# Kernel optimization log

Hardware: AMD Instinct MI355X
Metric: run time of the kernel (lower is better)

The kernel has to match this reference:

```python
import jax, jax.numpy as jnp
import numpy as np

HIDDEN = 1024
N_HEADS = 16
N_KV = 4
HEAD_DIM = HIDDEN // N_HEADS  # 64


def setup_inputs() -> dict:
    key = jax.random.key(0)
    ks = jax.random.split(key, 10)
    B, S, D = 2, 2048, HIDDEN
    s = 0.02
    return {
        "hidden_states": jax.random.normal(ks[0], (B, S, D), jnp.float32),
        "attention_mask": jnp.ones((B, S), jnp.float32),
        "Wq": jax.random.normal(ks[1], (D, N_HEADS * HEAD_DIM), jnp.float32) * s,
        "bq": jnp.zeros((N_HEADS * HEAD_DIM,), jnp.float32),
        "Wk": jax.random.normal(ks[2], (D, N_KV * HEAD_DIM), jnp.float32) * s,
        "bk": jnp.zeros((N_KV * HEAD_DIM,), jnp.float32),
        "Wv": jax.random.normal(ks[3], (D, N_KV * HEAD_DIM), jnp.float32) * s,
        "bv": jnp.zeros((N_KV * HEAD_DIM,), jnp.float32),
        "Wo": jax.random.normal(ks[4], (D, D), jnp.float32) * s,
        "bo": jnp.zeros((D,), jnp.float32),
    }


def _rope(x):
    # x: [B, H, S, Dh]; half-split RoPE as in the torch module
    S, Dh = x.shape[-2], x.shape[-1]
    inv_freq = 1.0 / (10000.0 ** (jnp.arange(0, Dh, 2, dtype=jnp.float32) / Dh))
    freqs = jnp.arange(S, dtype=jnp.float32)[:, None] * inv_freq[None, :]  # [S, Dh/2]
    cos, sin = jnp.cos(freqs), jnp.sin(freqs)
    x1, x2 = jnp.split(x, 2, axis=-1)
    return jnp.concatenate([x1 * cos - x2 * sin, x1 * sin + x2 * cos], axis=-1)


def reference(hidden_states, attention_mask, Wq, bq, Wk, bk, Wv, bv, Wo, bo):
    B, S, D = hidden_states.shape
    q = (hidden_states @ Wq + bq).reshape(B, S, N_HEADS, HEAD_DIM).transpose(0, 2, 1, 3)
    k = (hidden_states @ Wk + bk).reshape(B, S, N_KV, HEAD_DIM).transpose(0, 2, 1, 3)
    v = (hidden_states @ Wv + bv).reshape(B, S, N_KV, HEAD_DIM).transpose(0, 2, 1, 3)
    q = _rope(q)
    k = _rope(k)
    rep = N_HEADS // N_KV
    k = jnp.repeat(k, rep, axis=1)  # [B, H, S, Dh]
    v = jnp.repeat(v, rep, axis=1)
    bias = (1.0 - attention_mask[:, None, None, :]) * -1e9  # [B,1,1,S]
    scores = jnp.einsum("bhqd,bhkd->bhqk", q, k) / jnp.sqrt(jnp.float32(HEAD_DIM))
    attn = jax.nn.softmax(scores + bias, axis=-1)
    out = jnp.einsum("bhqk,bhkd->bhqd", attn, v)
    out = out.transpose(0, 2, 1, 3).reshape(B, S, D)
    return out @ Wo + bo
```

## Files before the change

kernel.cpp:

```cpp
#include <hip/hip_runtime.h>

typedef __bf16 bf16;
typedef __attribute__((ext_vector_type(8))) __bf16 bf16x8;
typedef __attribute__((ext_vector_type(4))) __bf16 bf16x4;
typedef __attribute__((ext_vector_type(4))) float f32x4;
typedef __attribute__((ext_vector_type(16))) float f32x16;
typedef __attribute__((ext_vector_type(4))) unsigned int uint4v;

#define LOG2E 1.44269504088896340736f
#define QSCALE 0.18033688011112042f

__device__ inline void tr_tile(const float* __restrict__ in, bf16* __restrict__ out,
                               int R, int C, int bx, int by, int tid) {
    __shared__ float t[32][33];
    int tx = tid & 31, ty = tid >> 5;
    int rbase = by * 32, cbase = bx * 32;
#pragma unroll
    for (int i = 0; i < 4; i++) {
        int r = ty + i * 8;
        t[r][tx] = in[(size_t)(rbase + r) * C + cbase + tx];
    }
    __syncthreads();
#pragma unroll
    for (int i = 0; i < 4; i++) {
        int r = ty + i * 8;
        out[(size_t)(cbase + r) * R + rbase + tx] = (bf16)t[tx][r];
    }
}

__global__ __launch_bounds__(256) void prep_k(const float* __restrict__ X,
                                              const float* __restrict__ Wq,
                                              const float* __restrict__ Wk,
                                              const float* __restrict__ Wv,
                                              const float* __restrict__ Wo,
                                              const float* __restrict__ mask,
                                              bf16* __restrict__ Xb,
                                              bf16* __restrict__ WqT,
                                              bf16* __restrict__ WkT,
                                              bf16* __restrict__ WvT,
                                              bf16* __restrict__ WoT,
                                              float2* __restrict__ rt,
                                              float* __restrict__ Mb,
                                              int* __restrict__ mflags) {
    int blk = blockIdx.x, tid = threadIdx.x;
    if (blk < 2048) {
        int idx = (blk * 256 + tid) * 8;
        float4 a = *(const float4*)(X + idx);
        float4 b = *(const float4*)(X + idx + 4);
        bf16 v[8] = {(bf16)a.x, (bf16)a.y, (bf16)a.z, (bf16)a.w,
                     (bf16)b.x, (bf16)b.y, (bf16)b.z, (bf16)b.w};
        *(uint4*)(Xb + idx) = *(const uint4*)v;
    } else if (blk < 3072) {
        int t = blk - 2048; tr_tile(Wq, WqT, 1024, 1024, t & 31, t >> 5, tid);
    } else if (blk < 3328) {
        int t = blk - 3072; tr_tile(Wk, WkT, 1024, 256, t & 7, t >> 3, tid);
    } else if (blk < 3584) {
        int t = blk - 3328; tr_tile(Wv, WvT, 1024, 256, t & 7, t >> 3, tid);
    } else if (blk < 4608) {
        int t = blk - 3584; tr_tile(Wo, WoT, 1024, 1024, t & 31, t >> 5, tid);
    } else if (blk < 4864) {
        int idx = (blk - 4608) * 256 + tid;
        int s = idx >> 5, i = idx & 31;
        float inv = exp2f(-0.41524100370589830f * (float)i);
        float ang = (float)s * inv;
        rt[idx] = make_float2(cosf(ang), sinf(ang));
    } else {
        __shared__ int sflag;
        int b = blk - 4864;
        if (tid == 0) sflag = 1;
        __syncthreads();
        const float* mrow = mask + (size_t)b * 2048;
        int i0 = tid * 8;
        bool ones = true;
#pragma unroll
        for (int j = 0; j < 8; j++) {
            float m = mrow[i0 + j];
            if (m != 1.0f) ones = false;
            Mb[(size_t)b * 2048 + i0 + j] = (1.0f - m) * (-1e9f) * LOG2E;
        }
        if (!ones) sflag = 0;
        __syncthreads();
        if (tid == 0) mflags[b] = sflag;
    }
}

__device__ __forceinline__ void gemm_main_db(bf16* __restrict__ pool,
                                             const bf16* __restrict__ A,
                                             const bf16* __restrict__ BT,
                                             int m0, int n0, int tid,
                                             f32x4 (&acc)[2][8]) {
    int w = tid >> 6, lane = tid & 63, l15 = lane & 15, quad = lane >> 4;

    int srow = lane >> 3;
    int kx = ((lane & 7) ^ srow) * 8;
    const bf16* ga0 = A + (size_t)(m0 + w * 32 + srow) * 1024 + kx;
    const bf16* gb0 = BT + (size_t)(n0 + w * 32 + srow) * 1024 + kx;
    int lofs = (w * 32) * 64 + lane * 8;

#define GSTAGE(K0, BUF)                                                                             \
    do {                                                                                            \
        bf16* gbase = pool + (BUF) * 16384;                                                         \
        _Pragma("unroll")                                                                           \
        for (int p = 0; p < 4; p++)                                                                 \
            __builtin_amdgcn_global_load_lds(                                                       \
                (const __attribute__((address_space(1))) unsigned int*)(ga0 + (size_t)p * 8 * 1024 + (K0)), \
                (__attribute__((address_space(3))) unsigned int*)(gbase + lofs + p * 512), 16, 0, 0); \
        _Pragma("unroll")                                                                           \
        for (int p = 0; p < 4; p++)                                                                 \
            __builtin_amdgcn_global_load_lds(                                                       \
                (const __attribute__((address_space(1))) unsigned int*)(gb0 + (size_t)p * 8 * 1024 + (K0)), \
                (__attribute__((address_space(3))) unsigned int*)(gbase + 8192 + lofs + p * 512), 16, 0, 0); \
    } while (0)

    GSTAGE(0, 0);
    __syncthreads();

    for (int ks = 0; ks < 16; ks++) {
        int cb = ks & 1;
        if (ks < 15) GSTAGE((ks + 1) * 64, cb ^ 1);
        const bf16* As = pool + cb * 16384;
        const bf16* Bs = As + 8192;
#pragma unroll
        for (int half = 0; half < 2; half++) {
            bf16x8 a[2], bfr[8];
            int kp = ((half * 4 + quad) ^ (l15 & 7)) * 8;
#pragma unroll
            for (int i = 0; i < 2; i++)
                a[i] = *(const bf16x8*)&As[(w * 32 + i * 16 + l15) * 64 + kp];
#pragma unroll
            for (int j = 0; j < 8; j++)
                bfr[j] = *(const bf16x8*)&Bs[(j * 16 + l15) * 64 + kp];
#pragma unroll
            for (int i = 0; i < 2; i++)
#pragma unroll
                for (int j = 0; j < 8; j++)
                    acc[i][j] = __builtin_amdgcn_mfma_f32_16x16x32_bf16(a[i], bfr[j], acc[i][j], 0, 0, 0);
        }
        __syncthreads();
    }
#undef GSTAGE
}

__global__ __launch_bounds__(256, 2) void qkv_gemm2(const bf16* __restrict__ Xb,
                                                    const bf16* __restrict__ WTall,
                                                    const float* __restrict__ bq,
                                                    const float* __restrict__ bk,
                                                    const float* __restrict__ bv,
                                                    const float2* __restrict__ rt,
                                                    bf16* __restrict__ Qb,
                                                    bf16* __restrict__ Kb,
                                                    bf16* __restrict__ VbT) {
    __shared__ __align__(16) bf16 pool[2 * 16384];
    int tt = blockIdx.x, gy = blockIdx.y, tid = threadIdx.x;
    f32x4 acc[2][8] = {};
    gemm_main_db(pool, Xb, WTall, tt * 128, gy * 128, tid, acc);

    int w = tid >> 6, lane = tid & 63, l15 = lane & 15, quad = lane >> 4;

    if (gy >= 10) {
        int kvb = (gy - 10) * 2;
        bf16* T = pool;
#pragma unroll
        for (int i = 0; i < 2; i++)
#pragma unroll
            for (int r = 0; r < 4; r++) {
                int s_local = w * 32 + i * 16 + quad * 4 + r;
#pragma unroll
                for (int j = 0; j < 8; j++) {
                    int dd = j * 16 + l15;
                    T[dd * 136 + s_local] = (bf16)(acc[i][j][r] + bv[kvb * 64 + dd]);
                }
            }
        __syncthreads();
        int dd = tid & 127, sblk = tid >> 7;
        int b = tt >> 4, s_base = (tt & 15) * 128 + sblk * 64;
        int head = kvb + (dd >> 6), d_in = dd & 63;
        const bf16* Trow = T + dd * 136 + sblk * 64;
        size_t orow = ((size_t)(b * 4 + head) * 64 + d_in) * 2048 + s_base;
#pragma unroll
        for (int c = 0; c < 8; c++)
            *(uint4*)(VbT + orow + c * 8) = *(const uint4*)(Trow + c * 8);
        return;
    }

    int mode = (gy < 8) ? 0 : 1;
#pragma unroll
    for (int jh = 0; jh < 2; jh++) {
        int head = (mode == 0) ? gy * 2 + jh : (gy - 8) * 2 + jh;
        const float* bias = ((mode == 0) ? bq : bk) + head * 64;
        bf16* dst = (mode == 0) ? Qb : Kb;
#pragma unroll
        for (int i = 0; i < 2; i++) {
#pragma unroll
            for (int r = 0; r < 4; r++) {
                int token = tt * 128 + w * 32 + i * 16 + quad * 4 + r;
                int b = token >> 11, s = token & 2047;
                float vals[4];
#pragma unroll
                for (int j = 0; j < 4; j++) vals[j] = acc[i][jh * 4 + j][r] + bias[j * 16 + l15];
#pragma unroll
                for (int c = 0; c < 2; c++) {
                    float2 cs2 = rt[s * 32 + c * 16 + l15];
                    float x1 = vals[c], x2 = vals[c + 2];
                    vals[c]     = x1 * cs2.x - x2 * cs2.y;
                    vals[c + 2] = x1 * cs2.y + x2 * cs2.x;
                }
                if (mode == 0) {
#pragma unroll
                    for (int j = 0; j < 4; j++) vals[j] *= QSCALE;
                }
                size_t base;
                if (mode == 0) base = (((size_t)b * 16 + head) * 2048 + s) * 64;
                else           base = (((size_t)b * 4  + head) * 2048 + s) * 64;
#pragma unroll
                for (int j = 0; j < 4; j++) dst[base + j * 16 + l15] = (bf16)vals[j];
            }
        }
    }
}

__global__ __launch_bounds__(256, 2) void oproj_gemm2(const bf16* __restrict__ Ab,
                                                      const bf16* __restrict__ WoT,
                                                      const float* __restrict__ bo,
                                                      float* __restrict__ out) {
    __shared__ __align__(16) bf16 pool[2 * 16384];
    int tt = blockIdx.x, nt = blockIdx.y, tid = threadIdx.x;
    f32x4 acc[2][8] = {};
    gemm_main_db(pool, Ab, WoT, tt * 128, nt * 128, tid, acc);

    int w = tid >> 6, lane = tid & 63, l15 = lane & 15, quad = lane >> 4;
#pragma unroll
    for (int i = 0; i < 2; i++) {
#pragma unroll
        for (int r = 0; r < 4; r++) {
            int token = tt * 128 + w * 32 + i * 16 + quad * 4 + r;
#pragma unroll
            for (int j = 0; j < 8; j++) {
                int n = nt * 128 + j * 16 + l15;
                out[(size_t)token * 1024 + n] = acc[i][j][r] + bo[n];
            }
        }
    }
}

__global__ __launch_bounds__(256, 4) void attn_k(const bf16* __restrict__ Qb,
                                                 const bf16* __restrict__ Kb,
                                                 const bf16* __restrict__ VbT,
                                                 const float* __restrict__ Mb,
                                                 const int* __restrict__ mflags,
                                                 bf16* __restrict__ Opb,
                                                 float* __restrict__ Lp) {
    int qt = blockIdx.x, h = blockIdx.y, z = blockIdx.z;
    int b = z >> 1, sp = z & 1;
    int kvh = h >> 2;
    int kt0 = sp * 16;

    __shared__ bf16 Ks[2][64 * 64];
    __shared__ bf16 Vs[2][64 * 64];

    int tid = threadIdx.x, w = tid >> 6, lane = tid & 63, l31 = lane & 31, hi = lane >> 5;

    const bool maskOnes = (mflags[b] != 0);

    bf16x8 qa[4];
    {
        size_t qrow = (((size_t)b * 16 + h) * 2048 + (size_t)qt * 128 + w * 32 + l31) * 64;
#pragma unroll
        for (int ds = 0; ds < 4; ds++)
            qa[ds] = *(const bf16x8*)(Qb + qrow + ds * 16 + hi * 8);
    }

    f32x16 oacc[2] = {};
    float lsum = 0.f;

    size_t kRow = ((size_t)b * 4 + kvh) * 2048;
    size_t vRow = ((size_t)b * 4 + kvh) * 64;

    int srow = lane >> 3;
    int kx = ((lane & 7) ^ srow) * 8;
    const bf16* gk0 = Kb + (kRow + w * 16 + srow) * 64 + kx;
    const bf16* gv0 = VbT + (vRow + w * 16 + srow) * 2048 + kx;
    int lofs = (w * 16) * 64 + lane * 8;

#define STAGE(KT, BUF)                                                                              \
    do {                                                                                            \
        _Pragma("unroll")                                                                           \
        for (int p = 0; p < 2; p++) {                                                               \
            __builtin_amdgcn_global_load_lds(                                                       \
                (const __attribute__((address_space(1))) unsigned int*)(gk0 + ((size_t)(KT) * 64 + p * 8) * 64), \
                (__attribute__((address_space(3))) unsigned int*)(&Ks[BUF][0] + lofs + p * 512), 16, 0, 0); \
            __builtin_amdgcn_global_load_lds(                                                       \
                (const __attribute__((address_space(1))) unsigned int*)(gv0 + (size_t)p * 8 * 2048 + (KT) * 64), \
                (__attribute__((address_space(3))) unsigned int*)(&Vs[BUF][0] + lofs + p * 512), 16, 0, 0); \
        }                                                                                           \
    } while (0)

    STAGE(kt0, 0);
    __syncthreads();

    const float* mbase = Mb + (size_t)b * 2048 + hi * 4;

    for (int kt = 0; kt < 16; kt++) {
        int cb = kt & 1;
        if (kt < 15) STAGE(kt0 + kt + 1, cb ^ 1);
        int ktg = kt0 + kt;

        const bf16* ksb = &Ks[cb][0];
        const bf16* vsb = &Vs[cb][0];

        uint4v paw[4];
#pragma unroll
        for (int kh = 0; kh < 2; kh++) {
            bf16x8 ka[4];
#pragma unroll
            for (int ds = 0; ds < 4; ds++) {
                int gran = ((ds * 2 + hi) ^ (l31 & 7)) * 8;
                ka[ds] = *(const bf16x8*)&ksb[(kh * 32 + l31) * 64 + gran];
            }
            f32x16 s = {};
#pragma unroll
            for (int ds = 0; ds < 4; ds++)
                s = __builtin_amdgcn_mfma_f32_32x32x16_bf16(ka[ds], qa[ds], s, 0, 0, 0);
            if (!maskOnes) {
#pragma unroll
                for (int g = 0; g < 4; g++) {
                    f32x4 b4 = *(const f32x4*)(mbase + ktg * 64 + kh * 32 + g * 8);
#pragma unroll
                    for (int r = 0; r < 4; r++) s[g * 4 + r] += b4[r];
                }
            }
#pragma unroll
            for (int i = 0; i < 16; i++) { s[i] = exp2f(s[i]); lsum += s[i]; }
            unsigned int d0, d1, d2, d3, d4, d5, d6, d7;
            asm("v_cvt_pk_bf16_f32 %0, %1, %2" : "=v"(d0) : "v"(s[0]),  "v"(s[1]));
            asm("v_cvt_pk_bf16_f32 %0, %1, %2" : "=v"(d1) : "v"(s[2]),  "v"(s[3]));
            asm("v_cvt_pk_bf16_f32 %0, %1, %2" : "=v"(d2) : "v"(s[4]),  "v"(s[5]));
            asm("v_cvt_pk_bf16_f32 %0, %1, %2" : "=v"(d3) : "v"(s[6]),  "v"(s[7]));
            asm("v_cvt_pk_bf16_f32 %0, %1, %2" : "=v"(d4) : "v"(s[8]),  "v"(s[9]));
            asm("v_cvt_pk_bf16_f32 %0, %1, %2" : "=v"(d5) : "v"(s[10]), "v"(s[11]));
            asm("v_cvt_pk_bf16_f32 %0, %1, %2" : "=v"(d6) : "v"(s[12]), "v"(s[13]));
            asm("v_cvt_pk_bf16_f32 %0, %1, %2" : "=v"(d7) : "v"(s[14]), "v"(s[15]));
            asm("v_permlane32_swap_b32 %0, %1" : "+v"(d0), "+v"(d2));
            asm("v_permlane32_swap_b32 %0, %1" : "+v"(d1), "+v"(d3));
            asm("v_permlane32_swap_b32 %0, %1" : "+v"(d4), "+v"(d6));
            asm("v_permlane32_swap_b32 %0, %1" : "+v"(d5), "+v"(d7));
            paw[kh * 2 + 0][0] = d0; paw[kh * 2 + 0][1] = d1;
            paw[kh * 2 + 0][2] = d2; paw[kh * 2 + 0][3] = d3;
            paw[kh * 2 + 1][0] = d4; paw[kh * 2 + 1][1] = d5;
            paw[kh * 2 + 1][2] = d6; paw[kh * 2 + 1][3] = d7;
        }

#pragma unroll
        for (int dg = 0; dg < 2; dg++)
#pragma unroll
            for (int ks = 0; ks < 4; ks++) {
                int gran = ((ks * 2 + hi) ^ (l31 & 7)) * 8;
                bf16x8 vb = *(const bf16x8*)&vsb[(dg * 32 + l31) * 64 + gran];
                oacc[dg] = __builtin_amdgcn_mfma_f32_32x32x16_bf16(
                    __builtin_bit_cast(bf16x8, paw[ks]), vb, oacc[dg], 0, 0, 0);
            }
        __syncthreads();
    }
#undef STAGE

    lsum += __shfl_xor(lsum, 32, 64);

#pragma unroll
    for (int dg = 0; dg < 2; dg++)
#pragma unroll
        for (int reg = 0; reg < 16; reg++) {
            int q = qt * 128 + w * 32 + (reg & 3) + 8 * (reg >> 2) + 4 * hi;
            Opb[((size_t)sp * 4096 + (size_t)b * 2048 + q) * 1024 + h * 64 + dg * 32 + l31] =
                (bf16)oacc[dg][reg];
        }
    if (hi == 0)
        Lp[((size_t)(sp * 2 + b) * 16 + h) * 2048 + qt * 128 + w * 32 + l31] = lsum;
}

__global__ __launch_bounds__(256) void merge_k(const bf16* __restrict__ Opb,
                                               const float* __restrict__ Lp,
                                               bf16* __restrict__ Ab) {
    int idx = (blockIdx.x * 256 + threadIdx.x) * 8;
    int tok = idx >> 10;
    int col = idx & 1023;
    int h = col >> 6;
    int b = tok >> 11, q = tok & 2047;
    float l0 = Lp[((size_t)b * 16 + h) * 2048 + q];
    float l1 = Lp[((size_t)(2 + b) * 16 + h) * 2048 + q];
    float inv = 1.0f / (l0 + l1);
    bf16x8 a = *(const bf16x8*)(Opb + idx);
    bf16x8 c = *(const bf16x8*)(Opb + (size_t)4096 * 1024 + idx);
    bf16 o[8];
#pragma unroll
    for (int j = 0; j < 8; j++) o[j] = (bf16)(((float)a[j] + (float)c[j]) * inv);
    *(uint4*)(Ab + idx) = *(const uint4*)o;
}

extern "C" void kernel_launch(void* const* d_in, const int* in_sizes, int n_in,
                              void* d_out, int out_size, void* d_ws, size_t ws_size,
                              hipStream_t stream) {
    const float* X    = (const float*)d_in[0];
    const float* mask = (const float*)d_in[1];
    const float* Wq   = (const float*)d_in[2];
    const float* bq   = (const float*)d_in[3];
    const float* Wk   = (const float*)d_in[4];
    const float* bk   = (const float*)d_in[5];
    const float* Wv   = (const float*)d_in[6];
    const float* bv   = (const float*)d_in[7];
    const float* Wo   = (const float*)d_in[8];
    const float* bo   = (const float*)d_in[9];
    float* out = (float*)d_out;
    bf16* ws  = (bf16*)d_ws;

    bf16* Xb  = ws;
    bf16* WqT = Xb + (size_t)4096 * 1024;
    bf16* WkT = WqT + 1024 * 1024;
    bf16* WvT = WkT + 256 * 1024;
    bf16* WoT = WvT + 256 * 1024;
    bf16* Qb  = WoT + 1024 * 1024;
    bf16* Kb  = Qb + (size_t)2 * 16 * 2048 * 64;
    bf16* VbT = Kb + (size_t)2 * 4 * 2048 * 64;
    bf16* Ab  = VbT + (size_t)2 * 4 * 2048 * 64;
    float2* rt = (float2*)(Ab + (size_t)2 * 2048 * 1024);
    float* Mb  = (float*)(rt + 2048 * 32);
    int* mflags = (int*)(Mb + 2 * 2048);
    bf16* Opb = (bf16*)(mflags + 4);
    float* Lp = (float*)(Opb + (size_t)2 * 4096 * 1024);

    prep_k<<<4866, 256, 0, stream>>>(X, Wq, Wk, Wv, Wo, mask, Xb, WqT, WkT, WvT, WoT, rt, Mb, mflags);
    qkv_gemm2<<<dim3(32, 12), 256, 0, stream>>>(Xb, WqT, bq, bk, bv, rt, Qb, Kb, VbT);
    attn_k<<<dim3(16, 16, 4), 256, 0, stream>>>(Qb, Kb, VbT, Mb, mflags, Opb, Lp);
    merge_k<<<2048, 256, 0, stream>>>(Opb, Lp, Ab);
    oproj_gemm2<<<dim3(32, 8), 256, 0, stream>>>(Ab, WoT, bo, out);
}
```

Measured before the change: 186.3 us.

## Replace double-buffered GEMM main loop with single-buffered loop for higher occupancy

The shared GEMM main loop goes from double-buffered async global-to-LDS staging to a single buffer that loads, syncs, computes and syncs again on each K step. LDS per block roughly halves, and launch bounds rise from 2 to 3 blocks per CU for the QKV and output-projection GEMMs. The goal is to hide memory latency through more resident blocks rather than intra-block prefetch. In exchange, each block now stalls on every load, and the tighter register budget may cause spills.

```diff
diff --git a/kernel.cpp b/kernel.cpp
--- a/kernel.cpp
+++ b/kernel.cpp
@@ -84,7 +84,7 @@
     }
 }
 
-__device__ __forceinline__ void gemm_main_db(bf16* __restrict__ pool,
+__device__ __forceinline__ void gemm_main_sb(bf16* __restrict__ pool,
                                              const bf16* __restrict__ A,
                                              const bf16* __restrict__ BT,
                                              int m0, int n0, int tid,
@@ -97,29 +97,20 @@
     const bf16* gb0 = BT + (size_t)(n0 + w * 32 + srow) * 1024 + kx;
     int lofs = (w * 32) * 64 + lane * 8;
 
-#define GSTAGE(K0, BUF)                                                                             \
-    do {                                                                                            \
-        bf16* gbase = pool + (BUF) * 16384;                                                         \
-        _Pragma("unroll")                                                                           \
-        for (int p = 0; p < 4; p++)                                                                 \
-            __builtin_amdgcn_global_load_lds(                                                       \
-                (const __attribute__((address_space(1))) unsigned int*)(ga0 + (size_t)p * 8 * 1024 + (K0)), \
-                (__attribute__((address_space(3))) unsigned int*)(gbase + lofs + p * 512), 16, 0, 0); \
-        _Pragma("unroll")                                                                           \
-        for (int p = 0; p < 4; p++)                                                                 \
-            __builtin_amdgcn_global_load_lds(                                                       \
-                (const __attribute__((address_space(1))) unsigned int*)(gb0 + (size_t)p * 8 * 1024 + (K0)), \
-                (__attribute__((address_space(3))) unsigned int*)(gbase + 8192 + lofs + p * 512), 16, 0, 0); \
-    } while (0)
-
-    GSTAGE(0, 0);
-    __syncthreads();
-
-    for (int ks = 0; ks < 16; ks++) {
-        int cb = ks & 1;
-        if (ks < 15) GSTAGE((ks + 1) * 64, cb ^ 1);
-        const bf16* As = pool + cb * 16384;
-        const bf16* Bs = As + 8192;
+    for (int k0 = 0; k0 < 1024; k0 += 64) {
+#pragma unroll
+        for (int p = 0; p < 4; p++)
+            __builtin_amdgcn_global_load_lds(
+                (const __attribute__((address_space(1))) unsigned int*)(ga0 + (size_t)p * 8 * 1024 + k0),
+                (__attribute__((address_space(3))) unsigned int*)(pool + lofs + p * 512), 16, 0, 0);
+#pragma unroll
+        for (int p = 0; p < 4; p++)
+            __builtin_amdgcn_global_load_lds(
+                (const __attribute__((address_space(1))) unsigned int*)(gb0 + (size_t)p * 8 * 1024 + k0),
+                (__attribute__((address_space(3))) unsigned int*)(pool + 8192 + lofs + p * 512), 16, 0, 0);
+        __syncthreads();
+        const bf16* As = pool;
+        const bf16* Bs = pool + 8192;
 #pragma unroll
         for (int half = 0; half < 2; half++) {
             bf16x8 a[2], bfr[8];
@@ -138,10 +129,9 @@
         }
         __syncthreads();
     }
-#undef GSTAGE
-}
-
-__global__ __launch_bounds__(256, 2) void qkv_gemm2(const bf16* __restrict__ Xb,
+}
+
+__global__ __launch_bounds__(256, 3) void qkv_gemm2(const bf16* __restrict__ Xb,
                                                     const bf16* __restrict__ WTall,
                                                     const float* __restrict__ bq,
                                                     const float* __restrict__ bk,
@@ -150,10 +140,10 @@
                                                     bf16* __restrict__ Qb,
                                                     bf16* __restrict__ Kb,
                                                     bf16* __restrict__ VbT) {
-    __shared__ __align__(16) bf16 pool[2 * 16384];
+    __shared__ __align__(16) bf16 pool[17408];
     int tt = blockIdx.x, gy = blockIdx.y, tid = threadIdx.x;
     f32x4 acc[2][8] = {};
-    gemm_main_db(pool, Xb, WTall, tt * 128, gy * 128, tid, acc);
+    gemm_main_sb(pool, Xb, WTall, tt * 128, gy * 128, tid, acc);
 
     int w = tid >> 6, lane = tid & 63, l15 = lane & 15, quad = lane >> 4;
 
@@ -219,14 +209,14 @@
     }
 }
 
-__global__ __launch_bounds__(256, 2) void oproj_gemm2(const bf16* __restrict__ Ab,
+__global__ __launch_bounds__(256, 3) void oproj_gemm2(const bf16* __restrict__ Ab,
                                                       const bf16* __restrict__ WoT,
                                                       const float* __restrict__ bo,
                                                       float* __restrict__ out) {
-    __shared__ __align__(16) bf16 pool[2 * 16384];
+    __shared__ __align__(16) bf16 pool[16384];
     int tt = blockIdx.x, nt = blockIdx.y, tid = threadIdx.x;
     f32x4 acc[2][8] = {};
-    gemm_main_db(pool, Ab, WoT, tt * 128, nt * 128, tid, acc);
+    gemm_main_sb(pool, Ab, WoT, tt * 128, nt * 128, tid, acc);
 
     int w = tid >> 6, lane = tid & 63, l15 = lane & 15, quad = lane >> 4;
 #pragma unroll
```

Result: slower. 191.1 us (+2.6%).
